# Kernel optimization log

Hardware: AMD Instinct MI355X
Metric: run time of the kernel (lower is better)

Reference implementation:

```python
import jax, jax.numpy as jnp
import numpy as np

NH = 16
D = 1024
DKH = D // NH  # 64


def _split_heads(x, nh):
    B, L, d = x.shape
    return x.reshape(B, L, nh, d // nh).transpose(0, 2, 1, 3)  # [B,Nh,L,dh]


def setup_inputs() -> dict:
    key = jax.random.key(0)
    ks = jax.random.split(key, 10)
    B, L, d = 2, 2048, D
    s = 1.0 / np.sqrt(d)
    inp = {
        "q": jax.random.normal(ks[0], (B, L, d), jnp.float32),
        "k": jax.random.normal(ks[1], (B, L, d), jnp.float32),
        "q_mask": jnp.ones((B, L), jnp.float32),
        "k_mask": jnp.ones((B, L), jnp.float32),
        "pos_logits": jax.random.normal(ks[2], (B, L, L), jnp.float32),
        # Linear params (torch convention: y = x @ W.T + b)
        "Wq": jax.random.normal(ks[3], (d, d), jnp.float32) * s,
        "bq": jnp.zeros((d,), jnp.float32),
        "Wk": jax.random.normal(ks[4], (d, d), jnp.float32) * s,
        "bk": jnp.zeros((d,), jnp.float32),
        "Wv": jax.random.normal(ks[5], (d, d), jnp.float32) * s,
        "bv": jnp.zeros((d,), jnp.float32),
        "Wo": jax.random.normal(ks[6], (d, d), jnp.float32) * s,
        "bo": jnp.zeros((d,), jnp.float32),
    }
    return inp


def reference(q, k, q_mask, k_mask, pos_logits, Wq, bq, Wk, bk, Wv, bv, Wo, bo):
    # Projections (note: v is computed from the *projected* k, as in the source)
    qp = (q @ Wq.T + bq) * (DKH ** -0.5)   # [B,Lq,dk]
    kp = k @ Wk.T + bk                     # [B,Lk,dk]
    vp = kp @ Wv.T + bv                    # [B,Lk,dv]

    qh = _split_heads(qp, NH)              # [B,Nh,Lq,dkh]
    kh = _split_heads(kp, NH)              # [B,Nh,Lk,dkh]
    vh = _split_heads(vp, NH)              # [B,Nh,Lk,dvh]

    # Additive attention mask: -inf where q_mask[i]*k_mask[j] == 0
    mask_prod = q_mask[:, :, None] * k_mask[:, None, :]          # [B,Lq,Lk]
    attn_mask = jnp.where(mask_prod == 0, jnp.float32(-jnp.inf), jnp.float32(0.0))[:, None]  # [B,1,Lq,Lk]

    con_logits = jnp.einsum("bhid,bhjd->bhij", qh, kh)           # [B,Nh,Lq,Lk]
    logits = attn_mask + con_logits + pos_logits[:, None]
    weights = jax.nn.softmax(logits, axis=-1)
    attn = jnp.einsum("bhij,bhjd->bhid", weights, vh)            # [B,Nh,Lq,dvh]

    B, Nh, Lq, dvh = attn.shape
    attn = attn.transpose(0, 2, 1, 3).reshape(B, Lq, Nh * dvh)   # combine heads
    out = attn @ Wo.T + bo                                       # output projection
    # dropout is identity in eval mode
    return out
```

## Files before the change

### kernel.cpp

```cpp
#include <hip/hip_runtime.h>
#include <math.h>

#define BB 2
#define LL 2048
#define DMODEL 1024
#define NHEAD 16
#define MTOK 4096
#define KVB 32
#define NT (LL / KVB)

typedef unsigned short u16;
typedef __attribute__((ext_vector_type(8))) short short8;
typedef __attribute__((ext_vector_type(4))) float f32x4;

__device__ __host__ inline u16 f2bf(float f) {
    unsigned u = __builtin_bit_cast(unsigned, f);
    return (u16)((u + 0x7FFFu + ((u >> 16) & 1u)) >> 16);
}
__device__ inline float bf2f(u16 h) {
    unsigned u = ((unsigned)h) << 16;
    return __builtin_bit_cast(float, u);
}

__global__ __launch_bounds__(256)
void split_planes(const float* __restrict__ x, u16* __restrict__ hi,
                  u16* __restrict__ lo, int n4)
{
    for (int i = blockIdx.x * blockDim.x + threadIdx.x; i < n4;
         i += gridDim.x * blockDim.x) {
        float4 v = ((const float4*)x)[i];
        ushort4 h, l;
        h.x = f2bf(v.x); l.x = f2bf(v.x - bf2f(h.x));
        h.y = f2bf(v.y); l.y = f2bf(v.y - bf2f(h.y));
        h.z = f2bf(v.z); l.z = f2bf(v.z - bf2f(h.z));
        h.w = f2bf(v.w); l.w = f2bf(v.w - bf2f(h.w));
        ((ushort4*)hi)[i] = h;
        ((ushort4*)lo)[i] = l;
    }
}

#define GBM 128
#define GBN 64
#define GBK 32

__global__ __launch_bounds__(256)
void gemm_mfma_split(const u16* __restrict__ Ahi, const u16* __restrict__ Alo,
                     const u16* __restrict__ Bhi, const u16* __restrict__ Blo,
                     const float* __restrict__ bias, float scale, int K, int N,
                     float* __restrict__ Yf, u16* __restrict__ Yhi,
                     u16* __restrict__ Ylo, int mode)
{
    __shared__ u16 lds[2][12288];

    const int tid = threadIdx.x;
    const int lid = tid & 63;
    const int w   = tid >> 6;
    const int wm  = w >> 1, wn = w & 1;
    const int m0  = blockIdx.y * GBM;
    const int n0  = blockIdx.x * GBN;

    f32x4 acc[4][2];
    #pragma unroll
    for (int ms = 0; ms < 4; ++ms)
        #pragma unroll
        for (int ns = 0; ns < 2; ++ns)
            acc[ms][ns] = (f32x4){0.f, 0.f, 0.f, 0.f};

    auto stage = [&](int buf, int t) {
        const int k0 = t * GBK;
        #pragma unroll
        for (int j = 0; j < 6; ++j) {
            const int q = w * 6 + j;
            const u16* plane; int ldsoff, c, R0;
            if (q < 8)       { plane = Ahi; ldsoff = 0;     c = q;      R0 = m0; }
            else if (q < 16) { plane = Alo; ldsoff = 4096;  c = q - 8;  R0 = m0; }
            else if (q < 20) { plane = Bhi; ldsoff = 8192;  c = q - 16; R0 = n0; }
            else             { plane = Blo; ldsoff = 10240; c = q - 20; R0 = n0; }
            const int r  = c * 16 + (lid >> 2);
            const int ci = lid & 3;
            const int kl = ci ^ ((r >> 1) & 3);
            const u16* g = plane + (size_t)(R0 + r) * K + k0 + kl * 8;
            __builtin_amdgcn_global_load_lds(
                (const __attribute__((address_space(1))) void*)g,
                (__attribute__((address_space(3))) void*)(&lds[buf][ldsoff + c * 512]),
                16, 0, 0);
        }
    };

    auto compute = [&](int buf) {
        const u16* L = lds[buf];
        short8 ah[4], al[4], bh[2], bl[2];
        #pragma unroll
        for (int ms = 0; ms < 4; ++ms) {
            const int r   = wm * 64 + ms * 16 + (lid & 15);
            const int off = r * 32 + (((lid >> 4) ^ ((r >> 1) & 3)) * 8);
            ah[ms] = *(const short8*)&L[off];
            al[ms] = *(const short8*)&L[4096 + off];
        }
        #pragma unroll
        for (int ns = 0; ns < 2; ++ns) {
            const int r   = wn * 32 + ns * 16 + (lid & 15);
            const int off = r * 32 + (((lid >> 4) ^ ((r >> 1) & 3)) * 8);
            bh[ns] = *(const short8*)&L[8192 + off];
            bl[ns] = *(const short8*)&L[10240 + off];
        }
        #pragma unroll
        for (int ms = 0; ms < 4; ++ms)
            #pragma unroll
            for (int ns = 0; ns < 2; ++ns) {
                acc[ms][ns] = __builtin_amdgcn_mfma_f32_16x16x32_bf16(al[ms], bh[ns], acc[ms][ns], 0, 0, 0);
                acc[ms][ns] = __builtin_amdgcn_mfma_f32_16x16x32_bf16(ah[ms], bl[ns], acc[ms][ns], 0, 0, 0);
                acc[ms][ns] = __builtin_amdgcn_mfma_f32_16x16x32_bf16(ah[ms], bh[ns], acc[ms][ns], 0, 0, 0);
            }
    };

    const int nt = K / GBK;
    stage(0, 0);
    __syncthreads();
    for (int t = 0; t < nt; ++t) {
        const int buf = t & 1;
        if (t + 1 < nt) stage(buf ^ 1, t + 1);
        compute(buf);
        __syncthreads();
    }

    const int orow = (lid >> 4) * 4;
    #pragma unroll
    for (int ms = 0; ms < 4; ++ms)
        #pragma unroll
        for (int ns = 0; ns < 2; ++ns) {
            const int col = n0 + wn * 32 + ns * 16 + (lid & 15);
            const float bcol = bias[col];
            #pragma unroll
            for (int i = 0; i < 4; ++i) {
                const int row = m0 + wm * 64 + ms * 16 + orow + i;
                const float y = (acc[ms][ns][i] + bcol) * scale;
                if (mode == 0) {
                    Yf[(size_t)row * N + col] = y;
                } else if (mode == 1) {
                    const size_t idx = (size_t)row * N + col;
                    const u16 hh = f2bf(y);
                    Yhi[idx] = hh;
                    Ylo[idx] = f2bf(y - bf2f(hh));
                } else {
                    const size_t idx = (size_t)col * MTOK + row;
                    const u16 hh = f2bf(y);
                    Yhi[idx] = hh;
                    Ylo[idx] = f2bf(y - bf2f(hh));
                }
            }
        }
}

__global__ __launch_bounds__(256, 2)
void attn_mfma2(const u16* __restrict__ qph, const u16* __restrict__ qpl,
                const u16* __restrict__ kph, const u16* __restrict__ kpl,
                const u16* __restrict__ vth, const u16* __restrict__ vtl,
                const float* __restrict__ qmask, const float* __restrict__ kmask,
                const float* __restrict__ pos,
                u16* __restrict__ ach, u16* __restrict__ acl)
{
    __shared__ float pp[4][1024];
    __shared__ u16  kvb[2][4][2048];

    const int tid = threadIdx.x;
    const int lid = tid & 63;
    const int w   = tid >> 6;
    const int q16 = lid & 15;
    const int hi4 = lid >> 4;
    const int qt = blockIdx.x, h = blockIdx.y, b = blockIdx.z;
    const int qw = qt * 128 + w * 32;

    short8 qh[2][2], ql[2][2];
    #pragma unroll
    for (int mf = 0; mf < 2; ++mf)
        #pragma unroll
        for (int ks = 0; ks < 2; ++ks) {
            const size_t off = (size_t)(b * LL + qw + mf * 16 + q16) * DMODEL
                             + h * 64 + ks * 32 + hi4 * 8;
            qh[mf][ks] = *(const short8*)(qph + off);
            ql[mf][ks] = *(const short8*)(qpl + off);
        }

    auto stage = [&](int buf, int t) {
        const int k0 = t * KVB;
        u16* dst = &kvb[buf][w][0];
        #pragma unroll
        for (int c = 0; c < 4; ++c) {
            const u16* src;
            if (w < 2) {
                const int r  = c * 8 + (lid >> 3);
                const int sl = (lid & 7) ^ (r & 7);
                src = (w == 0 ? kph : kpl) +
                      (size_t)(b * LL + k0 + r) * DMODEL + h * 64 + sl * 8;
            } else {
                const int r  = c * 16 + (lid >> 2);
                const int sl = (lid & 3) ^ ((r >> 1) & 3);
                src = (w == 2 ? vth : vtl) +
                      (size_t)(h * 64 + r) * MTOK + b * LL + k0 + sl * 8;
            }
            __builtin_amdgcn_global_load_lds(
                (const __attribute__((address_space(1))) void*)src,
                (__attribute__((address_space(3))) void*)(dst + c * 512), 16, 0, 0);
        }
    };

    float m_run[2] = {-INFINITY, -INFINITY};
    float l_run[2] = {0.f, 0.f};
    float qml[2];
    qml[0] = qmask[b * LL + qw + q16];
    qml[1] = qmask[b * LL + qw + 16 + q16];

    f32x4 o_acc[2][4];
    #pragma unroll
    for (int mf = 0; mf < 2; ++mf)
        #pragma unroll
        for (int nfd = 0; nfd < 4; ++nfd)
            o_acc[mf][nfd] = (f32x4){0.f, 0.f, 0.f, 0.f};

    stage(0, 0);
    __syncthreads();

    for (int t = 0; t < NT; ++t) {
        const int buf = t & 1;
        const int k0  = t * KVB;

        float4 kmv[2], posr[2][2];
        #pragma unroll
        for (int nf = 0; nf < 2; ++nf)
            kmv[nf] = *(const float4*)(kmask + b * LL + k0 + nf * 16 + hi4 * 4);
        #pragma unroll
        for (int mf = 0; mf < 2; ++mf)
            #pragma unroll
            for (int nf = 0; nf < 2; ++nf)
                posr[mf][nf] = *(const float4*)(pos +
                    ((size_t)(b * LL + qw + mf * 16 + q16)) * LL +
                    k0 + nf * 16 + hi4 * 4);

        if (t + 1 < NT) stage(buf ^ 1, t + 1);

        f32x4 s_acc[2][2];
        #pragma unroll
        for (int mf = 0; mf < 2; ++mf)
            #pragma unroll
            for (int nf = 0; nf < 2; ++nf)
                s_acc[mf][nf] = (f32x4){0.f, 0.f, 0.f, 0.f};

        #pragma unroll
        for (int ks = 0; ks < 2; ++ks)
            #pragma unroll
            for (int nf = 0; nf < 2; ++nf) {
                const int r  = nf * 16 + q16;
                const int sl = (ks * 4 + hi4) ^ (r & 7);
                short8 kbh = *(const short8*)(&kvb[buf][0][r * 64 + sl * 8]);
                short8 kbl = *(const short8*)(&kvb[buf][1][r * 64 + sl * 8]);
                #pragma unroll
                for (int mf = 0; mf < 2; ++mf) {
                    s_acc[mf][nf] = __builtin_amdgcn_mfma_f32_16x16x32_bf16(kbl, qh[mf][ks], s_acc[mf][nf], 0, 0, 0);
                    s_acc[mf][nf] = __builtin_amdgcn_mfma_f32_16x16x32_bf16(kbh, ql[mf][ks], s_acc[mf][nf], 0, 0, 0);
                    s_acc[mf][nf] = __builtin_amdgcn_mfma_f32_16x16x32_bf16(kbh, qh[mf][ks], s_acc[mf][nf], 0, 0, 0);
                }
            }

        #pragma unroll
        for (int mf = 0; mf < 2; ++mf) {
            float v[2][4];
            #pragma unroll
            for (int nf = 0; nf < 2; ++nf) {
                const float* km = (const float*)&kmv[nf];
                const float* pr = (const float*)&posr[mf][nf];
                #pragma unroll
                for (int i = 0; i < 4; ++i)
                    v[nf][i] = (qml[mf] * km[i] == 0.f)
                               ? -INFINITY : s_acc[mf][nf][i] + pr[i];
            }
            float rm = fmaxf(fmaxf(fmaxf(v[0][0], v[0][1]), fmaxf(v[0][2], v[0][3])),
                             fmaxf(fmaxf(v[1][0], v[1][1]), fmaxf(v[1][2], v[1][3])));
            rm = fmaxf(rm, __shfl_xor(rm, 16));
            rm = fmaxf(rm, __shfl_xor(rm, 32));
            const float mn = fmaxf(m_run[mf], rm);
            const float c  = __expf(m_run[mf] - mn);
            float ls = 0.f;
            float p[2][4];
            #pragma unroll
            for (int nf = 0; nf < 2; ++nf)
                #pragma unroll
                for (int i = 0; i < 4; ++i) {
                    p[nf][i] = __expf(v[nf][i] - mn);
                    ls += p[nf][i];
                }
            ls += __shfl_xor(ls, 16);
            ls += __shfl_xor(ls, 32);
            l_run[mf] = l_run[mf] * c + ls;
            m_run[mf] = mn;
            #pragma unroll
            for (int nfd = 0; nfd < 4; ++nfd)
                o_acc[mf][nfd] *= c;
            const int r = mf * 16 + q16;
            #pragma unroll
            for (int nf = 0; nf < 2; ++nf) {
                const int sl = (nf * 4 + hi4) ^ (r & 7);
                *(f32x4*)&pp[w][r * 32 + sl * 4] =
                    (f32x4){p[nf][0], p[nf][1], p[nf][2], p[nf][3]};
            }
        }

        short8 pah[2], pal[2];
        #pragma unroll
        for (int mf = 0; mf < 2; ++mf) {
            const int r  = mf * 16 + q16;
            const int s0 = (hi4 * 2)     ^ (r & 7);
            const int s1 = (hi4 * 2 + 1) ^ (r & 7);
            f32x4 pa = *(const f32x4*)&pp[w][r * 32 + s0 * 4];
            f32x4 pb = *(const f32x4*)&pp[w][r * 32 + s1 * 4];
            float f[8] = {pa[0], pa[1], pa[2], pa[3], pb[0], pb[1], pb[2], pb[3]};
            short8 hv, lv;
            #pragma unroll
            for (int jj = 0; jj < 8; ++jj) {
                const unsigned u = __builtin_bit_cast(unsigned, f[jj]);
                hv[jj] = (short)(u >> 16);
                const float lof = f[jj] - __builtin_bit_cast(float, u & 0xFFFF0000u);
                lv[jj] = (short)(__builtin_bit_cast(unsigned, lof) >> 16);
            }
            pah[mf] = hv; pal[mf] = lv;
        }
        #pragma unroll
        for (int nfd = 0; nfd < 4; ++nfd) {
            const int r  = nfd * 16 + q16;
            const int sl = hi4 ^ ((r >> 1) & 3);
            short8 vbh = *(const short8*)(&kvb[buf][2][r * 32 + sl * 8]);
            short8 vbl = *(const short8*)(&kvb[buf][3][r * 32 + sl * 8]);
            #pragma unroll
            for (int mf = 0; mf < 2; ++mf) {
                o_acc[mf][nfd] = __builtin_amdgcn_mfma_f32_16x16x32_bf16(vbl, pah[mf], o_acc[mf][nfd], 0, 0, 0);
                o_acc[mf][nfd] = __builtin_amdgcn_mfma_f32_16x16x32_bf16(vbh, pal[mf], o_acc[mf][nfd], 0, 0, 0);
                o_acc[mf][nfd] = __builtin_amdgcn_mfma_f32_16x16x32_bf16(vbh, pah[mf], o_acc[mf][nfd], 0, 0, 0);
            }
        }

        __syncthreads();
    }

    #pragma unroll
    for (int mf = 0; mf < 2; ++mf) {
        const float inv = 1.0f / l_run[mf];
        const size_t rb = (size_t)(b * LL + qw + mf * 16 + q16) * DMODEL + h * 64;
        #pragma unroll
        for (int nfd = 0; nfd < 4; ++nfd) {
            ushort4 hv, lv;
            #pragma unroll
            for (int i = 0; i < 4; ++i) {
                const float y  = o_acc[mf][nfd][i] * inv;
                const u16 hh   = f2bf(y);
                (&hv.x)[i] = hh;
                (&lv.x)[i] = f2bf(y - bf2f(hh));
            }
            *(ushort4*)(ach + rb + nfd * 16 + hi4 * 4) = hv;
            *(ushort4*)(acl + rb + nfd * 16 + hi4 * 4) = lv;
        }
    }
}

extern "C" void kernel_launch(void* const* d_in, const int* in_sizes, int n_in,
                              void* d_out, int out_size, void* d_ws, size_t ws_size,
                              hipStream_t stream)
{
    const float* q     = (const float*)d_in[0];
    const float* k     = (const float*)d_in[1];
    const float* qmask = (const float*)d_in[2];
    const float* kmask = (const float*)d_in[3];
    const float* pos   = (const float*)d_in[4];
    const float* Wq    = (const float*)d_in[5];
    const float* bq    = (const float*)d_in[6];
    const float* Wk    = (const float*)d_in[7];
    const float* bk    = (const float*)d_in[8];
    const float* Wv    = (const float*)d_in[9];
    const float* bv    = (const float*)d_in[10];
    const float* Wo    = (const float*)d_in[11];
    const float* bo    = (const float*)d_in[12];
    float* out = (float*)d_out;

    const size_t P  = (size_t)MTOK * DMODEL;
    const size_t PW = (size_t)DMODEL * DMODEL;

    u16* base = (u16*)d_ws;
    u16* qp_h = base;            u16* qp_l = qp_h + P;
    u16* kp_h = base + 2 * P;    u16* kp_l = kp_h + P;
    u16* bufA = base + 4 * P;
    u16* bufB = base + 6 * P;
    u16* wq_h = base + 8 * P;    u16* wq_l = wq_h + PW;
    u16* wk_h = wq_l + PW;       u16* wk_l = wk_h + PW;
    u16* wv_h = wk_l + PW;       u16* wv_l = wv_h + PW;
    u16* wo_h = wv_l + PW;       u16* wo_l = wo_h + PW;

    split_planes<<<1024, 256, 0, stream>>>(q,  bufA, bufA + P, (int)(P / 4));
    split_planes<<<1024, 256, 0, stream>>>(k,  bufB, bufB + P, (int)(P / 4));
    split_planes<<<512,  256, 0, stream>>>(Wq, wq_h, wq_l, (int)(PW / 4));
    split_planes<<<512,  256, 0, stream>>>(Wk, wk_h, wk_l, (int)(PW / 4));
    split_planes<<<512,  256, 0, stream>>>(Wv, wv_h, wv_l, (int)(PW / 4));
    split_planes<<<512,  256, 0, stream>>>(Wo, wo_h, wo_l, (int)(PW / 4));

    const dim3 gb(DMODEL / GBN, MTOK / GBM);
    const dim3 ga(LL / 128, NHEAD, BB);

    gemm_mfma_split<<<gb, 256, 0, stream>>>(bufA, bufA + P, wq_h, wq_l, bq, 0.125f,
                                            DMODEL, DMODEL, nullptr, qp_h, qp_l, 1);
    gemm_mfma_split<<<gb, 256, 0, stream>>>(bufB, bufB + P, wk_h, wk_l, bk, 1.0f,
                                            DMODEL, DMODEL, nullptr, kp_h, kp_l, 1);
    gemm_mfma_split<<<gb, 256, 0, stream>>>(kp_h, kp_l, wv_h, wv_l, bv, 1.0f,
                                            DMODEL, DMODEL, nullptr, bufA, bufA + P, 2);
    attn_mfma2<<<ga, 256, 0, stream>>>(qp_h, qp_l, kp_h, kp_l, bufA, bufA + P,
                                       qmask, kmask, pos, bufB, bufB + P);
    gemm_mfma_split<<<gb, 256, 0, stream>>>(bufB, bufB + P, wo_h, wo_l, bo, 1.0f,
                                            DMODEL, DMODEL, out, nullptr, nullptr, 0);
}
```

Before: 477.7 us.

## Halve attention query tile per wave, fuse split launches, vectorize transposed stores

The attention kernel now gives each wave 16 query rows instead of 32 and each block 64 queries, doubling the grid and allowing 4 blocks per CU. This trades K/V tile reuse for more parallelism and lower register pressure. The six plane-split launches are merged into two multi-tensor kernels to cut launch overhead. The transposed V-projection epilogue packs four bf16 values per lane into a single 8-byte store instead of scattered 2-byte stores.

```diff
diff --git a/kernel.cpp b/kernel.cpp
--- a/kernel.cpp
+++ b/kernel.cpp
@@ -22,9 +22,8 @@
     return __builtin_bit_cast(float, u);
 }
 
-__global__ __launch_bounds__(256)
-void split_planes(const float* __restrict__ x, u16* __restrict__ hi,
-                  u16* __restrict__ lo, int n4)
+__device__ inline void split_one(const float* __restrict__ x, u16* __restrict__ hi,
+                                 u16* __restrict__ lo, int n4)
 {
     for (int i = blockIdx.x * blockDim.x + threadIdx.x; i < n4;
          i += gridDim.x * blockDim.x) {
@@ -36,6 +35,30 @@
         h.w = f2bf(v.w); l.w = f2bf(v.w - bf2f(h.w));
         ((ushort4*)hi)[i] = h;
         ((ushort4*)lo)[i] = l;
+    }
+}
+
+__global__ __launch_bounds__(256)
+void split_planes2(const float* __restrict__ x0, u16* __restrict__ h0, u16* __restrict__ l0,
+                   const float* __restrict__ x1, u16* __restrict__ h1, u16* __restrict__ l1,
+                   int n4)
+{
+    if (blockIdx.y == 0) split_one(x0, h0, l0, n4);
+    else                 split_one(x1, h1, l1, n4);
+}
+
+__global__ __launch_bounds__(256)
+void split_planes4(const float* __restrict__ x0, u16* __restrict__ h0, u16* __restrict__ l0,
+                   const float* __restrict__ x1, u16* __restrict__ h1, u16* __restrict__ l1,
+                   const float* __restrict__ x2, u16* __restrict__ h2, u16* __restrict__ l2,
+                   const float* __restrict__ x3, u16* __restrict__ h3, u16* __restrict__ l3,
+                   int n4)
+{
+    switch (blockIdx.y & 3) {
+        case 0: split_one(x0, h0, l0, n4); break;
+        case 1: split_one(x1, h1, l1, n4); break;
+        case 2: split_one(x2, h2, l2, n4); break;
+        default: split_one(x3, h3, l3, n4); break;
     }
 }
 
@@ -131,36 +154,47 @@
         for (int ns = 0; ns < 2; ++ns) {
             const int col = n0 + wn * 32 + ns * 16 + (lid & 15);
             const float bcol = bias[col];
-            #pragma unroll
-            for (int i = 0; i < 4; ++i) {
-                const int row = m0 + wm * 64 + ms * 16 + orow + i;
-                const float y = (acc[ms][ns][i] + bcol) * scale;
-                if (mode == 0) {
-                    Yf[(size_t)row * N + col] = y;
-                } else if (mode == 1) {
-                    const size_t idx = (size_t)row * N + col;
+            if (mode == 2) {
+                const int r0 = m0 + wm * 64 + ms * 16 + orow;
+                unsigned ph[2] = {0, 0}, pl[2] = {0, 0};
+                #pragma unroll
+                for (int i = 0; i < 4; ++i) {
+                    const float y = (acc[ms][ns][i] + bcol) * scale;
                     const u16 hh = f2bf(y);
-                    Yhi[idx] = hh;
-                    Ylo[idx] = f2bf(y - bf2f(hh));
-                } else {
-                    const size_t idx = (size_t)col * MTOK + row;
-                    const u16 hh = f2bf(y);
-                    Yhi[idx] = hh;
-                    Ylo[idx] = f2bf(y - bf2f(hh));
+                    const u16 ll = f2bf(y - bf2f(hh));
+                    ph[i >> 1] |= ((unsigned)hh) << ((i & 1) * 16);
+                    pl[i >> 1] |= ((unsigned)ll) << ((i & 1) * 16);
                 }
-            }
-        }
-}
-
-__global__ __launch_bounds__(256, 2)
-void attn_mfma2(const u16* __restrict__ qph, const u16* __restrict__ qpl,
+                const size_t idx = (size_t)col * MTOK + r0;
+                *(uint2*)(Yhi + idx) = make_uint2(ph[0], ph[1]);
+                *(uint2*)(Ylo + idx) = make_uint2(pl[0], pl[1]);
+            } else {
+                #pragma unroll
+                for (int i = 0; i < 4; ++i) {
+                    const int row = m0 + wm * 64 + ms * 16 + orow + i;
+                    const float y = (acc[ms][ns][i] + bcol) * scale;
+                    if (mode == 0) {
+                        Yf[(size_t)row * N + col] = y;
+                    } else {
+                        const size_t idx = (size_t)row * N + col;
+                        const u16 hh = f2bf(y);
+                        Yhi[idx] = hh;
+                        Ylo[idx] = f2bf(y - bf2f(hh));
+                    }
+                }
+            }
+        }
+}
+
+__global__ __launch_bounds__(256, 4)
+void attn_mfma3(const u16* __restrict__ qph, const u16* __restrict__ qpl,
                 const u16* __restrict__ kph, const u16* __restrict__ kpl,
                 const u16* __restrict__ vth, const u16* __restrict__ vtl,
                 const float* __restrict__ qmask, const float* __restrict__ kmask,
                 const float* __restrict__ pos,
                 u16* __restrict__ ach, u16* __restrict__ acl)
 {
-    __shared__ float pp[4][1024];
+    __shared__ float pp[4][512];
     __shared__ u16  kvb[2][4][2048];
 
     const int tid = threadIdx.x;
@@ -169,18 +203,16 @@
     const int q16 = lid & 15;
     const int hi4 = lid >> 4;
     const int qt = blockIdx.x, h = blockIdx.y, b = blockIdx.z;
-    const int qw = qt * 128 + w * 32;
-
-    short8 qh[2][2], ql[2][2];
+    const int qw = qt * 64 + w * 16;
+
+    short8 qh[2], ql[2];
     #pragma unroll
-    for (int mf = 0; mf < 2; ++mf)
-        #pragma unroll
-        for (int ks = 0; ks < 2; ++ks) {
-            const size_t off = (size_t)(b * LL + qw + mf * 16 + q16) * DMODEL
-                             + h * 64 + ks * 32 + hi4 * 8;
-            qh[mf][ks] = *(const short8*)(qph + off);
-            ql[mf][ks] = *(const short8*)(qpl + off);
-        }
+    for (int ks = 0; ks < 2; ++ks) {
+        const size_t off = (size_t)(b * LL + qw + q16) * DMODEL
+                         + h * 64 + ks * 32 + hi4 * 8;
+        qh[ks] = *(const short8*)(qph + off);
+        ql[ks] = *(const short8*)(qpl + off);
+    }
 
     auto stage = [&](int buf, int t) {
         const int k0 = t * KVB;
@@ -205,18 +237,13 @@
         }
     };
 
-    float m_run[2] = {-INFINITY, -INFINITY};
-    float l_run[2] = {0.f, 0.f};
-    float qml[2];
-    qml[0] = qmask[b * LL + qw + q16];
-    qml[1] = qmask[b * LL + qw + 16 + q16];
-
-    f32x4 o_acc[2][4];
+    float m_run = -INFINITY, l_run = 0.f;
+    const float qml = qmask[b * LL + qw + q16];
+
+    f32x4 o_acc[4];
     #pragma unroll
-    for (int mf = 0; mf < 2; ++mf)
-        #pragma unroll
-        for (int nfd = 0; nfd < 4; ++nfd)
-            o_acc[mf][nfd] = (f32x4){0.f, 0.f, 0.f, 0.f};
+    for (int nfd = 0; nfd < 4; ++nfd)
+        o_acc[nfd] = (f32x4){0.f, 0.f, 0.f, 0.f};
 
     stage(0, 0);
     __syncthreads();
@@ -225,26 +252,19 @@
         const int buf = t & 1;
         const int k0  = t * KVB;
 
-        float4 kmv[2], posr[2][2];
-        #pragma unroll
-        for (int nf = 0; nf < 2; ++nf)
-            kmv[nf] = *(const float4*)(kmask + b * LL + k0 + nf * 16 + hi4 * 4);
-        #pragma unroll
-        for (int mf = 0; mf < 2; ++mf)
-            #pragma unroll
-            for (int nf = 0; nf < 2; ++nf)
-                posr[mf][nf] = *(const float4*)(pos +
-                    ((size_t)(b * LL + qw + mf * 16 + q16)) * LL +
-                    k0 + nf * 16 + hi4 * 4);
+        float4 kmv[2], posr[2];
+        #pragma unroll
+        for (int nf = 0; nf < 2; ++nf) {
+            kmv[nf]  = *(const float4*)(kmask + b * LL + k0 + nf * 16 + hi4 * 4);
+            posr[nf] = *(const float4*)(pos +
+                ((size_t)(b * LL + qw + q16)) * LL + k0 + nf * 16 + hi4 * 4);
+        }
 
         if (t + 1 < NT) stage(buf ^ 1, t + 1);
 
-        f32x4 s_acc[2][2];
-        #pragma unroll
-        for (int mf = 0; mf < 2; ++mf)
-            #pragma unroll
-            for (int nf = 0; nf < 2; ++nf)
-                s_acc[mf][nf] = (f32x4){0.f, 0.f, 0.f, 0.f};
+        f32x4 s_acc[2];
+        s_acc[0] = (f32x4){0.f, 0.f, 0.f, 0.f};
+        s_acc[1] = (f32x4){0.f, 0.f, 0.f, 0.f};
 
         #pragma unroll
         for (int ks = 0; ks < 2; ++ks)
@@ -254,32 +274,28 @@
                 const int sl = (ks * 4 + hi4) ^ (r & 7);
                 short8 kbh = *(const short8*)(&kvb[buf][0][r * 64 + sl * 8]);
                 short8 kbl = *(const short8*)(&kvb[buf][1][r * 64 + sl * 8]);
-                #pragma unroll
-                for (int mf = 0; mf < 2; ++mf) {
-                    s_acc[mf][nf] = __builtin_amdgcn_mfma_f32_16x16x32_bf16(kbl, qh[mf][ks], s_acc[mf][nf], 0, 0, 0);
-                    s_acc[mf][nf] = __builtin_amdgcn_mfma_f32_16x16x32_bf16(kbh, ql[mf][ks], s_acc[mf][nf], 0, 0, 0);
-                    s_acc[mf][nf] = __builtin_amdgcn_mfma_f32_16x16x32_bf16(kbh, qh[mf][ks], s_acc[mf][nf], 0, 0, 0);
-                }
-            }
-
-        #pragma unroll
-        for (int mf = 0; mf < 2; ++mf) {
+                s_acc[nf] = __builtin_amdgcn_mfma_f32_16x16x32_bf16(kbl, qh[ks], s_acc[nf], 0, 0, 0);
+                s_acc[nf] = __builtin_amdgcn_mfma_f32_16x16x32_bf16(kbh, ql[ks], s_acc[nf], 0, 0, 0);
+                s_acc[nf] = __builtin_amdgcn_mfma_f32_16x16x32_bf16(kbh, qh[ks], s_acc[nf], 0, 0, 0);
+            }
+
+        {
             float v[2][4];
             #pragma unroll
             for (int nf = 0; nf < 2; ++nf) {
                 const float* km = (const float*)&kmv[nf];
-                const float* pr = (const float*)&posr[mf][nf];
+                const float* pr = (const float*)&posr[nf];
                 #pragma unroll
                 for (int i = 0; i < 4; ++i)
-                    v[nf][i] = (qml[mf] * km[i] == 0.f)
-                               ? -INFINITY : s_acc[mf][nf][i] + pr[i];
+                    v[nf][i] = (qml * km[i] == 0.f)
+                               ? -INFINITY : s_acc[nf][i] + pr[i];
             }
             float rm = fmaxf(fmaxf(fmaxf(v[0][0], v[0][1]), fmaxf(v[0][2], v[0][3])),
                              fmaxf(fmaxf(v[1][0], v[1][1]), fmaxf(v[1][2], v[1][3])));
             rm = fmaxf(rm, __shfl_xor(rm, 16));
             rm = fmaxf(rm, __shfl_xor(rm, 32));
-            const float mn = fmaxf(m_run[mf], rm);
-            const float c  = __expf(m_run[mf] - mn);
+            const float mn = fmaxf(m_run, rm);
+            const float c  = __expf(m_run - mn);
             float ls = 0.f;
             float p[2][4];
             #pragma unroll
@@ -291,12 +307,12 @@
                 }
             ls += __shfl_xor(ls, 16);
             ls += __shfl_xor(ls, 32);
-            l_run[mf] = l_run[mf] * c + ls;
-            m_run[mf] = mn;
+            l_run = l_run * c + ls;
+            m_run = mn;
             #pragma unroll
             for (int nfd = 0; nfd < 4; ++nfd)
-                o_acc[mf][nfd] *= c;
-            const int r = mf * 16 + q16;
+                o_acc[nfd] *= c;
+            const int r = q16;
             #pragma unroll
             for (int nf = 0; nf < 2; ++nf) {
                 const int sl = (nf * 4 + hi4) ^ (r & 7);
@@ -305,24 +321,21 @@
             }
         }
 
-        short8 pah[2], pal[2];
-        #pragma unroll
-        for (int mf = 0; mf < 2; ++mf) {
-            const int r  = mf * 16 + q16;
+        short8 pah, pal;
+        {
+            const int r  = q16;
             const int s0 = (hi4 * 2)     ^ (r & 7);
             const int s1 = (hi4 * 2 + 1) ^ (r & 7);
             f32x4 pa = *(const f32x4*)&pp[w][r * 32 + s0 * 4];
             f32x4 pb = *(const f32x4*)&pp[w][r * 32 + s1 * 4];
             float f[8] = {pa[0], pa[1], pa[2], pa[3], pb[0], pb[1], pb[2], pb[3]};
-            short8 hv, lv;
             #pragma unroll
             for (int jj = 0; jj < 8; ++jj) {
                 const unsigned u = __builtin_bit_cast(unsigned, f[jj]);
-                hv[jj] = (short)(u >> 16);
+                pah[jj] = (short)(u >> 16);
                 const float lof = f[jj] - __builtin_bit_cast(float, u & 0xFFFF0000u);
-                lv[jj] = (short)(__builtin_bit_cast(unsigned, lof) >> 16);
-            }
-            pah[mf] = hv; pal[mf] = lv;
+                pal[jj] = (short)(__builtin_bit_cast(unsigned, lof) >> 16);
+            }
         }
         #pragma unroll
         for (int nfd = 0; nfd < 4; ++nfd) {
@@ -330,27 +343,23 @@
             const int sl = hi4 ^ ((r >> 1) & 3);
             short8 vbh = *(const short8*)(&kvb[buf][2][r * 32 + sl * 8]);
             short8 vbl = *(const short8*)(&kvb[buf][3][r * 32 + sl * 8]);
-            #pragma unroll
-            for (int mf = 0; mf < 2; ++mf) {
-                o_acc[mf][nfd] = __builtin_amdgcn_mfma_f32_16x16x32_bf16(vbl, pah[mf], o_acc[mf][nfd], 0, 0, 0);
-                o_acc[mf][nfd] = __builtin_amdgcn_mfma_f32_16x16x32_bf16(vbh, pal[mf], o_acc[mf][nfd], 0, 0, 0);
-                o_acc[mf][nfd] = __builtin_amdgcn_mfma_f32_16x16x32_bf16(vbh, pah[mf], o_acc[mf][nfd], 0, 0, 0);
-            }
+            o_acc[nfd] = __builtin_amdgcn_mfma_f32_16x16x32_bf16(vbl, pah, o_acc[nfd], 0, 0, 0);
+            o_acc[nfd] = __builtin_amdgcn_mfma_f32_16x16x32_bf16(vbh, pal, o_acc[nfd], 0, 0, 0);
+            o_acc[nfd] = __builtin_amdgcn_mfma_f32_16x16x32_bf16(vbh, pah, o_acc[nfd], 0, 0, 0);
         }
 
         __syncthreads();
     }
 
-    #pragma unroll
-    for (int mf = 0; mf < 2; ++mf) {
-        const float inv = 1.0f / l_run[mf];
-        const size_t rb = (size_t)(b * LL + qw + mf * 16 + q16) * DMODEL + h * 64;
+    {
+        const float inv = 1.0f / l_run;
+        const size_t rb = (size_t)(b * LL + qw + q16) * DMODEL + h * 64;
         #pragma unroll
         for (int nfd = 0; nfd < 4; ++nfd) {
             ushort4 hv, lv;
             #pragma unroll
             for (int i = 0; i < 4; ++i) {
-                const float y  = o_acc[mf][nfd][i] * inv;
+                const float y  = o_acc[nfd][i] * inv;
                 const u16 hh   = f2bf(y);
                 (&hv.x)[i] = hh;
                 (&lv.x)[i] = f2bf(y - bf2f(hh));
@@ -393,15 +402,14 @@
     u16* wv_h = wk_l + PW;       u16* wv_l = wv_h + PW;
     u16* wo_h = wv_l + PW;       u16* wo_l = wo_h + PW;
 
-    split_planes<<<1024, 256, 0, stream>>>(q,  bufA, bufA + P, (int)(P / 4));
-    split_planes<<<1024, 256, 0, stream>>>(k,  bufB, bufB + P, (int)(P / 4));
-    split_planes<<<512,  256, 0, stream>>>(Wq, wq_h, wq_l, (int)(PW / 4));
-    split_planes<<<512,  256, 0, stream>>>(Wk, wk_h, wk_l, (int)(PW / 4));
-    split_planes<<<512,  256, 0, stream>>>(Wv, wv_h, wv_l, (int)(PW / 4));
-    split_planes<<<512,  256, 0, stream>>>(Wo, wo_h, wo_l, (int)(PW / 4));
+    split_planes2<<<dim3(1024, 2), 256, 0, stream>>>(
+        q, bufA, bufA + P, k, bufB, bufB + P, (int)(P / 4));
+    split_planes4<<<dim3(512, 4), 256, 0, stream>>>(
+        Wq, wq_h, wq_l, Wk, wk_h, wk_l, Wv, wv_h, wv_l, Wo, wo_h, wo_l,
+        (int)(PW / 4));
 
     const dim3 gb(DMODEL / GBN, MTOK / GBM);
-    const dim3 ga(LL / 128, NHEAD, BB);
+    const dim3 ga(LL / 64, NHEAD, BB);
 
     gemm_mfma_split<<<gb, 256, 0, stream>>>(bufA, bufA + P, wq_h, wq_l, bq, 0.125f,
                                             DMODEL, DMODEL, nullptr, qp_h, qp_l, 1);
@@ -409,7 +417,7 @@
                                             DMODEL, DMODEL, nullptr, kp_h, kp_l, 1);
     gemm_mfma_split<<<gb, 256, 0, stream>>>(kp_h, kp_l, wv_h, wv_l, bv, 1.0f,
                                             DMODEL, DMODEL, nullptr, bufA, bufA + P, 2);
-    attn_mfma2<<<ga, 256, 0, stream>>>(qp_h, qp_l, kp_h, kp_l, bufA, bufA + P,
+    attn_mfma3<<<ga, 256, 0, stream>>>(qp_h, qp_l, kp_h, kp_l, bufA, bufA + P,
                                        qmask, kmask, pos, bufB, bufB + P);
     gemm_mfma_split<<<gb, 256, 0, stream>>>(bufB, bufB + P, wo_h, wo_l, bo, 1.0f,
                                             DMODEL, DMODEL, out, nullptr, nullptr, 0);
```

After: 470.1 us. No clear change (-1.6%).
